# Kernel optimization log

Measured on AMD Instinct MI355X. Metric: run time of the kernel, lower is better.

## Reference

```python
import jax, jax.numpy as jnp
import numpy as np

D = 1024      # d_model
E = 8         # num_experts
K = 2         # top_k
H = 4096      # expert_dim (bottleneck)
P = 256       # proj_dim
BATCH, SEQ = 2, 2048
CLAMP_MAX = float(np.log(1.0 / 0.01))
INIT_T = 0.5


def setup_inputs() -> dict:
    key = jax.random.key(0)
    ks = jax.random.split(key, 6)
    x = jax.random.normal(ks[0], (BATCH, SEQ, D), jnp.float32)
    # cosine projector (nn.Linear default init ~ U(-1/sqrt(D), 1/sqrt(D)))
    lim = 1.0 / np.sqrt(D)
    Wp = jax.random.uniform(ks[1], (P, D), jnp.float32, -lim, lim)
    bp = jnp.zeros((P,), jnp.float32)
    sim = 0.01 * jax.random.normal(ks[2], (P, E), jnp.float32)
    temp = jnp.full((1,), np.log(1.0 / INIT_T), jnp.float32)
    # RepAdapter 1x1 convs == linear layers; xavier_uniform, zero bias
    bA = float(np.sqrt(6.0 / (D + H)))
    A = jax.random.uniform(ks[3], (E, H, D), jnp.float32, -bA, bA)
    a_bias = jnp.zeros((E, H), jnp.float32)
    Bw = jax.random.uniform(ks[4], (E, D, H), jnp.float32, -bA, bA)
    b_bias = jnp.zeros((E, D), jnp.float32)
    return dict(x=x, Wp=Wp, bp=bp, sim=sim, temp=temp, A=A, a_bias=a_bias, Bw=Bw, b_bias=b_bias)


def reference(x, Wp, bp, sim, temp, A, a_bias, Bw, b_bias):
    B, S, d = x.shape
    e = sim.shape[1]
    xf = x.reshape(-1, d)                                  # [T, D]
    # cosine gate
    proj = xf @ Wp.T + bp                                  # [T, P]
    projn = proj / jnp.maximum(jnp.linalg.norm(proj, axis=1, keepdims=True), 1e-12)
    simn = sim / jnp.maximum(jnp.linalg.norm(sim, axis=0, keepdims=True), 1e-12)
    scale = jnp.exp(jnp.minimum(temp, CLAMP_MAX))          # [1]
    gate_probs = jax.nn.softmax((projn @ simn) * scale, axis=-1)   # [T, E]
    topv, topi = jax.lax.top_k(gate_probs, K)              # [T, K]
    topv = topv / (topv.sum(axis=-1, keepdims=True) + 1e-8)
    # per-token per-expert combine weight
    w = jnp.sum(topv[:, :, None] * jax.nn.one_hot(topi, e, dtype=x.dtype), axis=1)  # [T, E]

    # experts: y_e(x) = x + B_e(A_e x + a_e) + b_e (no nonlinearity); combine weighted
    def body(acc, params):
        Ae, ab, Be, bb, we = params
        h = xf @ Ae.T + ab                                 # [T, H]
        f = h @ Be.T + bb                                  # [T, D]
        return acc + we[:, None] * (xf + f), None

    out, _ = jax.lax.scan(body, jnp.zeros_like(xf), (A, a_bias, Bw, b_bias, w.T))
    out = out.reshape(B, S, d)

    frac = gate_probs.mean(axis=0)                         # expert_fractions
    aux_loss = jnp.sum((frac - 1.0 / e) ** 2)
    usage = jnp.bincount(topi.reshape(-1), length=e).astype(jnp.float32)
    return out, aux_loss, frac, usage
```

## Files before the change

kernel.cpp:

```cpp
#include <hip/hip_runtime.h>
#include <stdint.h>


typedef __attribute__((ext_vector_type(4))) float floatx4;
typedef __attribute__((ext_vector_type(8))) short shortx8;
typedef unsigned short ushort_t;

#define T_TOKENS 4096
#define D_DIM    1024
#define E_EXP    8
#define H_DIM    4096
#define P_DIM    256
#define ROWS_PAD 9344
#define MBLK     73

__device__ __forceinline__ ushort_t f2bf(float f) {
  union { float f; unsigned int u; } c; c.f = f;
  unsigned int u = c.u;
  unsigned int r = u + 0x7FFFu + ((u >> 16) & 1u);
  return (ushort_t)(r >> 16);
}

__device__ __forceinline__ void stage16(const ushort_t* g, ushort_t* l) {
  __builtin_amdgcn_global_load_lds(
      (__attribute__((address_space(1))) void*)(uintptr_t)g,
      (__attribute__((address_space(3))) void*)l, 16, 0, 0);
}

__global__ __launch_bounds__(256) void k_cvt(const float* __restrict__ src,
                                             ushort_t* __restrict__ dst, int n4) {
  int g = blockIdx.x * 256 + threadIdx.x;
  if (g >= n4) return;
  floatx4 v = ((const floatx4*)src)[g];
  ushort4 o; o.x = f2bf(v.x); o.y = f2bf(v.y); o.z = f2bf(v.z); o.w = f2bf(v.w);
  ((ushort4*)dst)[g] = o;
}

__global__ __launch_bounds__(256) void k_small_init(int* counts, int* cursor,
                                                    float* frac_sum, int* row2tok) {
  int g = blockIdx.x * 256 + threadIdx.x;
  if (g < 8) { counts[g] = 0; cursor[g] = 0; frac_sum[g] = 0.f; }
  if (g < ROWS_PAD) row2tok[g] = -1;
}

__global__ __launch_bounds__(256) void k_proj(const float* __restrict__ x,
                                              const float* __restrict__ Wp,
                                              const float* __restrict__ bp,
                                              float* __restrict__ proj) {
  __shared__ float Wc[256 * 36];
  __shared__ float Xc[16 * 36];
  int tid = threadIdx.x;
  int t0 = blockIdx.x * 16;
  int cg = tid & 31, tg = tid >> 5;
  floatx4 acc[2][8];
#pragma unroll
  for (int a = 0; a < 2; a++)
#pragma unroll
    for (int b = 0; b < 8; b++) acc[a][b] = (floatx4){0.f, 0.f, 0.f, 0.f};
  for (int kc = 0; kc < 32; ++kc) {
    int k0 = kc * 32;
    __syncthreads();
#pragma unroll
    for (int it = 0; it < 8; ++it) {
      int f = it * 256 + tid;
      int j = f >> 3, kk = (f & 7) << 2;
      floatx4 v = *(const floatx4*)(Wp + j * 1024 + k0 + kk);
      *(floatx4*)(Wc + j * 36 + kk) = v;
    }
    if (tid < 128) {
      int t = tid >> 3, kk = (tid & 7) << 2;
      floatx4 v = *(const floatx4*)(x + (size_t)(t0 + t) * 1024 + k0 + kk);
      *(floatx4*)(Xc + t * 36 + kk) = v;
    }
    __syncthreads();
#pragma unroll
    for (int k4 = 0; k4 < 8; ++k4) {
      floatx4 xv[2], wv[8];
#pragma unroll
      for (int tt = 0; tt < 2; tt++) xv[tt] = *(floatx4*)(Xc + (tg * 2 + tt) * 36 + k4 * 4);
#pragma unroll
      for (int jj = 0; jj < 8; jj++) wv[jj] = *(floatx4*)(Wc + (cg + jj * 32) * 36 + k4 * 4);
#pragma unroll
      for (int tt = 0; tt < 2; tt++)
#pragma unroll
        for (int jj = 0; jj < 8; jj++) acc[tt][jj] += xv[tt] * wv[jj];
    }
  }
#pragma unroll
  for (int tt = 0; tt < 2; tt++)
#pragma unroll
    for (int jj = 0; jj < 8; jj++) {
      floatx4 a = acc[tt][jj];
      float s = (a.x + a.y) + (a.z + a.w);
      int t = t0 + tg * 2 + tt, j = cg + jj * 32;
      proj[t * 256 + j] = s + bp[j];
    }
}

__global__ __launch_bounds__(128) void k_gate(const float* __restrict__ proj,
                                              const float* __restrict__ sim,
                                              const float* __restrict__ temp,
                                              int* __restrict__ topi, float* __restrict__ wslot,
                                              float* __restrict__ swsum,
                                              float* __restrict__ frac_sum, int* __restrict__ counts) {
  __shared__ float simT[8][256];
  __shared__ float snorm[8];
  __shared__ float fracs[8];
  __shared__ int cnts[8];
  int tid = threadIdx.x;
  for (int i = tid; i < 2048; i += 128) { int p = i >> 3, e = i & 7; simT[e][p] = sim[i]; }
  if (tid < 8) { fracs[tid] = 0.f; cnts[tid] = 0; }
  __syncthreads();
  if (tid < 8) {
    float s = 0.f;
    for (int p = 0; p < 256; p++) { float v = simT[tid][p]; s += v * v; }
    snorm[tid] = fmaxf(sqrtf(s), 1e-12f);
  }
  __syncthreads();
  int t = blockIdx.x * 128 + tid;
  floatx4 n4 = (floatx4){0.f, 0.f, 0.f, 0.f};
  floatx4 d4[8];
#pragma unroll
  for (int e = 0; e < 8; e++) d4[e] = (floatx4){0.f, 0.f, 0.f, 0.f};
  const floatx4* pr = (const floatx4*)(proj + t * 256);
  for (int k4 = 0; k4 < 64; ++k4) {
    floatx4 p = pr[k4];
    n4 += p * p;
#pragma unroll
    for (int e = 0; e < 8; e++) d4[e] += p * *(const floatx4*)(&simT[e][k4 * 4]);
  }
  float nrm = fmaxf(sqrtf((n4.x + n4.y) + (n4.z + n4.w)), 1e-12f);
  float scale = expf(fminf(temp[0], 4.6051701859880914f));
  float pe[8];
  float mx = -1e30f;
#pragma unroll
  for (int e = 0; e < 8; e++) {
    float d = (d4[e].x + d4[e].y) + (d4[e].z + d4[e].w);
    pe[e] = d / (nrm * snorm[e]) * scale;
    mx = fmaxf(mx, pe[e]);
  }
  float sum = 0.f;
#pragma unroll
  for (int e = 0; e < 8; e++) { pe[e] = expf(pe[e] - mx); sum += pe[e]; }
#pragma unroll
  for (int e = 0; e < 8; e++) pe[e] /= sum;
  int i0 = 0;
#pragma unroll
  for (int e = 1; e < 8; e++) if (pe[e] > pe[i0]) i0 = e;
  int i1 = (i0 == 0) ? 1 : 0;
#pragma unroll
  for (int e = 0; e < 8; e++) if (e != i1 && e != i0 && pe[e] > pe[i1]) i1 = e;
  float v0 = pe[i0], v1 = pe[i1];
  float s2 = v0 + v1 + 1e-8f;
  float w0 = v0 / s2, w1 = v1 / s2;
  topi[t * 2] = i0; topi[t * 2 + 1] = i1;
  wslot[t * 2] = w0; wslot[t * 2 + 1] = w1;
  swsum[t] = w0 + w1;
#pragma unroll
  for (int e = 0; e < 8; e++) atomicAdd(&fracs[e], pe[e]);
  atomicAdd(&cnts[i0], 1); atomicAdd(&cnts[i1], 1);
  __syncthreads();
  if (tid < 8) { atomicAdd(&frac_sum[tid], fracs[tid]); atomicAdd(&counts[tid], cnts[tid]); }
}

__global__ void k_scan(const int* __restrict__ counts, const float* __restrict__ frac_sum,
                       int* __restrict__ offsets, int* __restrict__ blk2e,
                       float* __restrict__ out_tail) {
  __shared__ int offs[9];
  if (threadIdx.x == 0) {
    int off = 0;
    for (int e = 0; e < 8; e++) { offs[e] = off; off += ((counts[e] + 127) >> 7) << 7; }
    offs[8] = off;
    for (int e = 0; e < 9; e++) offsets[e] = offs[e];
    float aux = 0.f;
    for (int e = 0; e < 8; e++) { float fr = frac_sum[e] / 4096.f; aux += (fr - 0.125f) * (fr - 0.125f); }
    out_tail[0] = aux;
  }
  __syncthreads();
  int tid = threadIdx.x;
  if (tid < MBLK) {
    int r = tid * 128, e = -1;
    for (int q = 0; q < 8; q++) if (r >= offs[q] && r < offs[q + 1]) e = q;
    blk2e[tid] = e;
  }
  if (tid < 8) {
    out_tail[1 + tid] = frac_sum[tid] / 4096.f;
    out_tail[9 + tid] = (float)counts[tid];
  }
}

__global__ __launch_bounds__(256) void k_assign(const int* __restrict__ topi,
                                                const float* __restrict__ wslot,
                                                const int* __restrict__ offsets,
                                                int* __restrict__ cursor,
                                                int* __restrict__ row2tok, float* __restrict__ roww) {
  int g = blockIdx.x * 256 + threadIdx.x;
  if (g >= 8192) return;
  int t = g >> 1;
  int e = topi[g];
  int pos = atomicAdd(&cursor[e], 1);
  int r = offsets[e] + pos;
  row2tok[r] = t;
  roww[r] = wslot[g];
}

__global__ __launch_bounds__(64) void k_gather(const float* __restrict__ x,
                                               const int* __restrict__ row2tok,
                                               ushort_t* __restrict__ xg) {
  int r = blockIdx.x;
  int t = row2tok[r];
  ushort4* dst = (ushort4*)(xg + (size_t)r * 1024);
  if (t < 0) {
    ushort4 z; z.x = z.y = z.z = z.w = 0;
    for (int i = threadIdx.x; i < 256; i += 64) dst[i] = z;
  } else {
    const floatx4* src = (const floatx4*)(x + (size_t)t * 1024);
    for (int i = threadIdx.x; i < 256; i += 64) {
      floatx4 v = src[i];
      ushort4 o; o.x = f2bf(v.x); o.y = f2bf(v.y); o.z = f2bf(v.z); o.w = f2bf(v.w);
      dst[i] = o;
    }
  }
}

__global__ __launch_bounds__(256) void k_init_out(const float* __restrict__ x,
                                                  const float* __restrict__ swsum,
                                                  float* __restrict__ out) {
  int g = blockIdx.x * 256 + threadIdx.x;
  float s = swsum[g >> 8];
  floatx4 v = ((const floatx4*)x)[g];
  ((floatx4*)out)[g] = v * s;
}

__global__ __launch_bounds__(256) void k_gemm(const ushort_t* __restrict__ Aop0,
                                              const ushort_t* __restrict__ Wall,
                                              const float* __restrict__ bias,
                                              const int* __restrict__ blk2e,
                                              int K, int N,
                                              ushort_t* __restrict__ hout,
                                              float* __restrict__ outp,
                                              const int* __restrict__ row2tok,
                                              const float* __restrict__ roww) {
  int e = blk2e[blockIdx.y];
  if (e < 0) return;
  int rb = blockIdx.y, nb = blockIdx.x;
  int Kslice = K / gridDim.z;
  int kbase = blockIdx.z * Kslice;
  const ushort_t* Aop = Aop0 + (size_t)rb * 128 * K + kbase;
  const ushort_t* Bop = Wall + (size_t)e * N * K + (size_t)nb * 128 * K + kbase;
  __shared__ ushort_t As[8192], Bs[8192];
  int tid = threadIdx.x, lane = tid & 63, wv = tid >> 6;
  int l15 = lane & 15, q = lane >> 4;
  int wm = (wv & 1) << 6, wn = (wv >> 1) << 6;
  floatx4 acc[4][4];
#pragma unroll
  for (int i = 0; i < 4; i++)
#pragma unroll
    for (int j = 0; j < 4; j++) acc[i][j] = (floatx4){0.f, 0.f, 0.f, 0.f};
  int row0 = tid >> 3;
  int swz  = (tid & 7) ^ (row0 & 7);
  size_t sa = (size_t)row0 * K + (size_t)(swz << 3);
  int ldsoff = wv * 512;
  int ksteps = Kslice >> 6;
  for (int ks = 0; ks < ksteps; ++ks) {
    const ushort_t* Ak = Aop + ks * 64;
    const ushort_t* Bk = Bop + ks * 64;
#pragma unroll
    for (int r = 0; r < 4; ++r) {
      stage16(Ak + sa + (size_t)(r * 32) * K, As + r * 2048 + ldsoff);
      stage16(Bk + sa + (size_t)(r * 32) * K, Bs + r * 2048 + ldsoff);
    }
    __syncthreads();
#pragma unroll
    for (int s = 0; s < 2; ++s) {
      int cw = (s << 2) + q;
      shortx8 af[4], bfv[4];
#pragma unroll
      for (int i = 0; i < 4; i++) {
        int row = wm + i * 16 + l15;
        af[i] = *(const shortx8*)(As + (row << 6) + ((cw ^ (row & 7)) << 3));
      }
#pragma unroll
      for (int j = 0; j < 4; j++) {
        int row = wn + j * 16 + l15;
        bfv[j] = *(const shortx8*)(Bs + (row << 6) + ((cw ^ (row & 7)) << 3));
      }
#pragma unroll
      for (int i = 0; i < 4; i++)
#pragma unroll
        for (int j = 0; j < 4; j++)
          acc[i][j] = __builtin_amdgcn_mfma_f32_16x16x32_bf16(af[i], bfv[j], acc[i][j], 0, 0, 0);
    }
    __syncthreads();
  }
  const float* be = bias + (size_t)e * N + (size_t)nb * 128;
  if (hout) {
    ushort_t* hp = hout + (size_t)(rb * 128) * N + nb * 128;
#pragma unroll
    for (int j = 0; j < 4; j++) {
      int n = wn + j * 16 + l15;
      float bv = be[n];
#pragma unroll
      for (int i = 0; i < 4; i++)
#pragma unroll
        for (int r = 0; r < 4; r++) {
          int m = wm + i * 16 + (q << 2) + r;
          hp[(size_t)m * N + n] = f2bf(acc[i][j][r] + bv);
        }
    }
  } else {
    bool addb = (blockIdx.z == 0);
#pragma unroll
    for (int j = 0; j < 4; j++) {
      int n = wn + j * 16 + l15;
      float bv = addb ? be[n] : 0.f;
#pragma unroll
      for (int i = 0; i < 4; i++)
#pragma unroll
        for (int r = 0; r < 4; r++) {
          int m = wm + i * 16 + (q << 2) + r;
          int grow = rb * 128 + m;
          int tok = row2tok[grow];
          if (tok >= 0) {
            float v = (acc[i][j][r] + bv) * roww[grow];
            atomicAdd(outp + (size_t)tok * 1024 + nb * 128 + n, v);
          }
        }
    }
  }
}

extern "C" void kernel_launch(void* const* d_in, const int* in_sizes, int n_in,
                              void* d_out, int out_size, void* d_ws, size_t ws_size,
                              hipStream_t stream) {
  (void)in_sizes; (void)n_in; (void)out_size; (void)ws_size;
  const float* x      = (const float*)d_in[0];
  const float* Wp     = (const float*)d_in[1];
  const float* bp     = (const float*)d_in[2];
  const float* sim    = (const float*)d_in[3];
  const float* temp   = (const float*)d_in[4];
  const float* A      = (const float*)d_in[5];
  const float* a_bias = (const float*)d_in[6];
  const float* Bw     = (const float*)d_in[7];
  const float* b_bias = (const float*)d_in[8];
  float* out = (float*)d_out;

  char* ws = (char*)d_ws;
  ushort_t* Abf    = (ushort_t*)(ws);
  ushort_t* Bbf    = (ushort_t*)(ws + 67108864);
  ushort_t* xg     = (ushort_t*)(ws + 134217728);
  ushort_t* h      = (ushort_t*)(ws + 153354240);
  float*    proj   = (float*)   (ws + 229900288);
  int*      topi   = (int*)     (ws + 234094592);
  float*    wslot  = (float*)   (ws + 234127360);
  float*    swsum  = (float*)   (ws + 234160128);
  int*      row2tok= (int*)     (ws + 234176512);
  float*    roww   = (float*)   (ws + 234213888);
  int*      counts = (int*)     (ws + 234251264);
  int*      cursor = (int*)     (ws + 234251296);
  int*      offsets= (int*)     (ws + 234251328);
  int*      blk2e  = (int*)     (ws + 234251392);
  float*    fracs  = (float*)   (ws + 234251712);

  k_cvt<<<32768, 256, 0, stream>>>(A,  Abf, 8388608);
  k_cvt<<<32768, 256, 0, stream>>>(Bw, Bbf, 8388608);
  k_small_init<<<37, 256, 0, stream>>>(counts, cursor, fracs, row2tok);
  k_proj<<<256, 256, 0, stream>>>(x, Wp, bp, proj);
  k_gate<<<32, 128, 0, stream>>>(proj, sim, temp, topi, wslot, swsum, fracs, counts);
  k_scan<<<1, 128, 0, stream>>>(counts, fracs, offsets, blk2e, out + 4194304);
  k_assign<<<32, 256, 0, stream>>>(topi, wslot, offsets, cursor, row2tok, roww);
  k_gather<<<ROWS_PAD, 64, 0, stream>>>(x, row2tok, xg);
  k_init_out<<<4096, 256, 0, stream>>>(x, swsum, out);
  k_gemm<<<dim3(32, MBLK, 1), 256, 0, stream>>>(xg, Abf, a_bias, blk2e, 1024, 4096,
                                                h, nullptr, nullptr, nullptr);
  k_gemm<<<dim3(8, MBLK, 4), 256, 0, stream>>>(h, Bbf, b_bias, blk2e, 4096, 1024,
                                               nullptr, out, row2tok, roww);
}
```

Baseline: 857.4 us.

## Register-prefetch next K tile in GEMM instead of direct global-to-LDS loads

Replaces the global_load_lds staging in the expert GEMM with register loads that are issued for the next K step right after the barrier, then written to swizzled LDS at the top of the following iteration. This overlaps global memory latency with the MFMA work of the current tile. It also halves the split-K factor of the second GEMM from 4 to 2, which means fewer atomic partial-sum writes to the output but fewer blocks in flight. The cost is extra VGPRs for the prefetch buffers and an explicit LDS write pass.

```diff
diff --git a/kernel.cpp b/kernel.cpp
--- a/kernel.cpp
+++ b/kernel.cpp
@@ -19,12 +19,6 @@
   unsigned int u = c.u;
   unsigned int r = u + 0x7FFFu + ((u >> 16) & 1u);
   return (ushort_t)(r >> 16);
-}
-
-__device__ __forceinline__ void stage16(const ushort_t* g, ushort_t* l) {
-  __builtin_amdgcn_global_load_lds(
-      (__attribute__((address_space(1))) void*)(uintptr_t)g,
-      (__attribute__((address_space(3))) void*)l, 16, 0, 0);
 }
 
 __global__ __launch_bounds__(256) void k_cvt(const float* __restrict__ src,
@@ -257,20 +251,33 @@
   for (int i = 0; i < 4; i++)
 #pragma unroll
     for (int j = 0; j < 4; j++) acc[i][j] = (floatx4){0.f, 0.f, 0.f, 0.f};
-  int row0 = tid >> 3;
-  int swz  = (tid & 7) ^ (row0 & 7);
-  size_t sa = (size_t)row0 * K + (size_t)(swz << 3);
-  int ldsoff = wv * 512;
+
+  int row0 = tid >> 3, colc = tid & 7;
+  size_t ga = (size_t)row0 * K + (size_t)(colc << 3);
+  int wa = (row0 << 6) + ((colc ^ (row0 & 7)) << 3);
   int ksteps = Kslice >> 6;
+
+  shortx8 rA[4], rB[4];
+#pragma unroll
+  for (int r = 0; r < 4; ++r) {
+    rA[r] = *(const shortx8*)(Aop + ga + (size_t)(r * 32) * K);
+    rB[r] = *(const shortx8*)(Bop + ga + (size_t)(r * 32) * K);
+  }
   for (int ks = 0; ks < ksteps; ++ks) {
-    const ushort_t* Ak = Aop + ks * 64;
-    const ushort_t* Bk = Bop + ks * 64;
 #pragma unroll
     for (int r = 0; r < 4; ++r) {
-      stage16(Ak + sa + (size_t)(r * 32) * K, As + r * 2048 + ldsoff);
-      stage16(Bk + sa + (size_t)(r * 32) * K, Bs + r * 2048 + ldsoff);
+      *(shortx8*)(As + wa + r * 2048) = rA[r];
+      *(shortx8*)(Bs + wa + r * 2048) = rB[r];
     }
     __syncthreads();
+    int kn = (ks + 1 < ksteps) ? (ks + 1) : ks;
+    const ushort_t* An = Aop + kn * 64;
+    const ushort_t* Bn = Bop + kn * 64;
+#pragma unroll
+    for (int r = 0; r < 4; ++r) {
+      rA[r] = *(const shortx8*)(An + ga + (size_t)(r * 32) * K);
+      rB[r] = *(const shortx8*)(Bn + ga + (size_t)(r * 32) * K);
+    }
 #pragma unroll
     for (int s = 0; s < 2; ++s) {
       int cw = (s << 2) + q;
@@ -373,6 +380,6 @@
   k_init_out<<<4096, 256, 0, stream>>>(x, swsum, out);
   k_gemm<<<dim3(32, MBLK, 1), 256, 0, stream>>>(xg, Abf, a_bias, blk2e, 1024, 4096,
                                                 h, nullptr, nullptr, nullptr);
-  k_gemm<<<dim3(8, MBLK, 4), 256, 0, stream>>>(h, Bbf, b_bias, blk2e, 4096, 1024,
+  k_gemm<<<dim3(8, MBLK, 2), 256, 0, stream>>>(h, Bbf, b_bias, blk2e, 4096, 1024,
                                                nullptr, out, row2tok, roww);
 }
```

After: 808.8 us. 5.7% less time.
